# Performance work log

Measured on AMD Instinct MI355X. Metric: run time of the kernel, lower is better.

Reference implementation:

```python
import jax, jax.numpy as jnp
import numpy as np

WINDOW = 4
EPS = 1e-5


def setup_inputs() -> dict:
    key = jax.random.key(0)
    ks = jax.random.split(key, 12)
    B, T, D = 2, 4096, 1024
    H = D // 2
    s = 0.02
    return {
        "x": jax.random.normal(ks[0], (B, T, D), dtype=jnp.float32),
        # tension_net: Linear(2D -> D/2), SiLU, Linear(D/2 -> 1). Weights stored [in, out].
        "w1": jax.random.normal(ks[1], (2 * D, H), dtype=jnp.float32) * s,
        "b1": jnp.zeros((H,), dtype=jnp.float32),
        "w2": jax.random.normal(ks[2], (H, 1), dtype=jnp.float32) * s,
        "b2": jnp.zeros((1,), dtype=jnp.float32),
        # wv: Linear(D -> D)
        "wv_w": jax.random.normal(ks[3], (D, D), dtype=jnp.float32) * s,
        "wv_b": jnp.zeros((D,), dtype=jnp.float32),
        # merge: Linear(2D -> D)
        "merge_w": jax.random.normal(ks[4], (2 * D, D), dtype=jnp.float32) * s,
        "merge_b": jnp.zeros((D,), dtype=jnp.float32),
        # LayerNorm(D)
        "gamma": jnp.ones((D,), dtype=jnp.float32),
        "beta": jnp.zeros((D,), dtype=jnp.float32),
    }


def reference(x, w1, b1, w2, b2, wv_w, wv_b, merge_w, merge_b, gamma, beta):
    B, T, D = x.shape
    W = WINDOW
    # Causal sliding-window neighbor gather: nb[:, t, w] = x[:, t-w-1] if t-w-1 >= 0 else 0.
    idx = jnp.arange(T)[:, None] - jnp.arange(W)[None, :] - 1          # [T, W]
    valid = (idx >= 0)                                                  # [T, W]
    nb = jnp.take(x, jnp.clip(idx, 0, None), axis=1)                   # [B, T, W, D]
    nb = jnp.where(valid[None, :, :, None], nb, jnp.zeros((), x.dtype))
    # Pairwise tension gate: tiny MLP on [h_t, nb].
    h_t = jnp.broadcast_to(x[:, :, None, :], (B, T, W, D))
    pair = jnp.concatenate([h_t, nb], axis=-1)                          # [B, T, W, 2D]
    hid = jax.nn.silu(jnp.einsum('btwe,eh->btwh', pair, w1) + b1)       # [B, T, W, D/2]
    tau = jax.nn.sigmoid((jnp.einsum('btwh,ho->btwo', hid, w2) + b2)[..., 0])  # [B, T, W]
    # Value projection of neighbors (note: zero-padded neighbors still get wv bias, matching torch).
    v = jnp.einsum('btwd,de->btwe', nb, wv_w) + wv_b                    # [B, T, W, D]
    msg = jnp.einsum('btw,btwd->btd', tau, v)                           # [B, T, D]
    # Merge + LayerNorm.
    y = jnp.einsum('bte,ed->btd', jnp.concatenate([x, msg], axis=-1), merge_w) + merge_b
    mu = jnp.mean(y, axis=-1, keepdims=True)
    var = jnp.mean(jnp.square(y - mu), axis=-1, keepdims=True)
    y = (y - mu) * jax.lax.rsqrt(var + EPS) * gamma + beta
    return y
```

## Files before the change

### kernel.cpp

```cpp
#include <hip/hip_runtime.h>
#include <hip/hip_bf16.h>

#define TT 4096
#define TD 1024
#define TH 512
#define TM 8192
#define EPS 1e-5f

typedef __bf16 bf16;
typedef __bf16 bf16x2 __attribute__((ext_vector_type(2)));
typedef __bf16 bf16x4 __attribute__((ext_vector_type(4)));
typedef __bf16 bf16x8 __attribute__((ext_vector_type(8)));
typedef float  f32x4  __attribute__((ext_vector_type(4)));

#define GLOBAL_AS __attribute__((address_space(1)))
#define LDS_AS    __attribute__((address_space(3)))

__global__ __launch_bounds__(256) void cast_x_kernel(const float4* __restrict__ x4,
                                                     bf16* __restrict__ XM) {
    int i = blockIdx.x * 256 + threadIdx.x;
    float4 v = x4[i];
    int row = i >> 8;
    int c4  = i & 255;
    bf16x4 o;
    o[0] = (bf16)v.x; o[1] = (bf16)v.y; o[2] = (bf16)v.z; o[3] = (bf16)v.w;
    *(bf16x4*)(XM + (size_t)row * 2048 + c4 * 4) = o;
}

__global__ __launch_bounds__(256) void transpose_w1wv(const float* __restrict__ w1,
                                                      const float* __restrict__ wv,
                                                      bf16* __restrict__ dst) {
    __shared__ float tile[32][33];
    const int z = blockIdx.z;
    const float* src; int N, dstOff;
    if (z == 0)      { src = w1;                      N = 512;  dstOff = 0;    }
    else if (z == 1) { src = w1 + (size_t)1024 * 512; N = 512;  dstOff = 512;  }
    else             { src = wv;                      N = 1024; dstOff = 1024; }
    int n0 = blockIdx.x * 32, k0 = blockIdx.y * 32;
    if (n0 >= N) return;
    int tx = threadIdx.x & 31, ty = threadIdx.x >> 5;
#pragma unroll
    for (int r = 0; r < 32; r += 8)
        tile[ty + r][tx] = src[(size_t)(k0 + ty + r) * N + n0 + tx];
    __syncthreads();
#pragma unroll
    for (int r = 0; r < 32; r += 8)
        dst[(size_t)(dstOff + n0 + ty + r) * 1024 + k0 + tx] = (bf16)tile[tx][ty + r];
}

__global__ __launch_bounds__(256) void transpose_merge(const float* __restrict__ src,
                                                       bf16* __restrict__ dst) {
    __shared__ float tile[32][33];
    int n0 = blockIdx.x * 32, k0 = blockIdx.y * 32;
    int tx = threadIdx.x & 31, ty = threadIdx.x >> 5;
#pragma unroll
    for (int r = 0; r < 32; r += 8)
        tile[ty + r][tx] = src[(size_t)(k0 + ty + r) * 1024 + n0 + tx];
    __syncthreads();
#pragma unroll
    for (int r = 0; r < 32; r += 8)
        dst[(size_t)(n0 + ty + r) * 2048 + k0 + tx] = (bf16)tile[tx][ty + r];
}

template <typename OutT>
__global__ __launch_bounds__(256) void gemm_bt(const bf16* __restrict__ A, int lda,
                                               const bf16* __restrict__ BT,
                                               OutT* __restrict__ C, int N, int K) {
    __shared__ bf16 As[128 * 64];
    __shared__ bf16 Bs[128 * 64];
    const int m0 = blockIdx.y * 128;
    const int n0 = blockIdx.x * 128;
    const int tid = threadIdx.x;
    const int wave = tid >> 6, lane = tid & 63;
    const int wr = (wave >> 1) * 64, wc = (wave & 1) * 64;
    const int lrow = lane & 15, cbase = lane >> 4;
    const int sw = lrow & 7;

    f32x4 acc[4][4] = {};

    for (int k0 = 0; k0 < K; k0 += 64) {
        __syncthreads();
#pragma unroll
        for (int c = 0; c < 4; ++c) {
            int e = (c * 256 + tid) * 8;
            int row = e >> 6;
            int q = (e >> 3) & 7;
            int gcol = ((q ^ (row & 7)) << 3);
            const bf16* ga = A  + (size_t)(m0 + row) * lda + k0 + gcol;
            const bf16* gb = BT + (size_t)(n0 + row) * K   + k0 + gcol;
            __builtin_amdgcn_global_load_lds((const GLOBAL_AS void*)ga,
                                             (LDS_AS void*)(As + e), 16, 0, 0);
            __builtin_amdgcn_global_load_lds((const GLOBAL_AS void*)gb,
                                             (LDS_AS void*)(Bs + e), 16, 0, 0);
        }
        __syncthreads();

#pragma unroll
        for (int kk = 0; kk < 2; ++kk) {
            const int qo = ((cbase + kk * 4) ^ sw) << 3;
            bf16x8 af[4], bfr[4];
#pragma unroll
            for (int i = 0; i < 4; ++i) {
                af[i]  = *(const bf16x8*)(As + (wr + i * 16 + lrow) * 64 + qo);
                bfr[i] = *(const bf16x8*)(Bs + (wc + i * 16 + lrow) * 64 + qo);
            }
#pragma unroll
            for (int i = 0; i < 4; ++i)
#pragma unroll
                for (int j = 0; j < 4; ++j)
                    acc[i][j] = __builtin_amdgcn_mfma_f32_16x16x32_bf16(af[i], bfr[j], acc[i][j], 0, 0, 0);
        }
    }

    const int lr = (lane >> 4) * 4, lc = lane & 15;
#pragma unroll
    for (int i = 0; i < 4; ++i)
#pragma unroll
        for (int j = 0; j < 4; ++j)
#pragma unroll
            for (int r = 0; r < 4; ++r)
                C[(size_t)(m0 + wr + i * 16 + lr + r) * N + (n0 + wc + j * 16 + lc)]
                    = (OutT)acc[i][j][r];
}

__global__ __launch_bounds__(256) void taumsg_kernel(const bf16* __restrict__ UVV,
                                                     const float* __restrict__ b1,
                                                     const float* __restrict__ b2,
                                                     const float* __restrict__ w2,
                                                     const float* __restrict__ wv_b,
                                                     bf16* __restrict__ XM) {
    const int row = blockIdx.x;
    const int t = row & (TT - 1);
    const int tid = threadIdx.x;

    const int h = tid * 2;
    bf16x2 ub = *(const bf16x2*)(UVV + (size_t)row * 2048 + h);
    float u0 = (float)ub[0] + b1[h];
    float u1 = (float)ub[1] + b1[h + 1];
    const float w20 = w2[h], w21 = w2[h + 1];

    float partial[4];
#pragma unroll
    for (int w = 0; w < 4; ++w) {
        float vn0 = 0.f, vn1 = 0.f;
        if (t >= w + 1) {
            bf16x2 vb = *(const bf16x2*)(UVV + (size_t)(row - w - 1) * 2048 + 512 + h);
            vn0 = (float)vb[0]; vn1 = (float)vb[1];
        }
        float z0 = u0 + vn0, z1 = u1 + vn1;
        float h0 = z0 / (1.f + __expf(-z0));
        float h1 = z1 / (1.f + __expf(-z1));
        partial[w] = h0 * w20 + h1 * w21;
    }
#pragma unroll
    for (int w = 0; w < 4; ++w)
        for (int off = 32; off; off >>= 1)
            partial[w] += __shfl_down(partial[w], off, 64);

    __shared__ float red[4][4];
    __shared__ float staus[4];
    const int lane = tid & 63, wave = tid >> 6;
    if (lane == 0)
#pragma unroll
        for (int w = 0; w < 4; ++w) red[w][wave] = partial[w];
    __syncthreads();
    if (tid < 4) {
        float s = red[tid][0] + red[tid][1] + red[tid][2] + red[tid][3] + b2[0];
        staus[tid] = 1.f / (1.f + __expf(-s));
    }
    __syncthreads();
    const float tau0 = staus[0], tau1 = staus[1], tau2 = staus[2], tau3 = staus[3];
    const float tsum = tau0 + tau1 + tau2 + tau3;

    const int d0 = tid * 4;
    float4 wb = *(const float4*)(wv_b + d0);
    float m[4] = {tsum * wb.x, tsum * wb.y, tsum * wb.z, tsum * wb.w};
    const float taus[4] = {tau0, tau1, tau2, tau3};
#pragma unroll
    for (int w = 0; w < 4; ++w) {
        if (t >= w + 1) {
            bf16x4 v = *(const bf16x4*)(UVV + (size_t)(row - w - 1) * 2048 + 1024 + d0);
#pragma unroll
            for (int j = 0; j < 4; ++j) m[j] += taus[w] * (float)v[j];
        }
    }
    bf16x4 o;
#pragma unroll
    for (int j = 0; j < 4; ++j) o[j] = (bf16)m[j];
    *(bf16x4*)(XM + (size_t)row * 2048 + 1024 + d0) = o;
}

__global__ __launch_bounds__(256) void ln_kernel(const bf16* __restrict__ Y,
                                                 const float* __restrict__ merge_b,
                                                 const float* __restrict__ gamma,
                                                 const float* __restrict__ beta,
                                                 float* __restrict__ out) {
    const int row = blockIdx.x;
    const int tid = threadIdx.x;
    const int d0 = tid * 4;
    bf16x4 y4 = *(const bf16x4*)(Y + (size_t)row * TD + d0);
    float4 mb = *(const float4*)(merge_b + d0);
    float v[4] = {(float)y4[0] + mb.x, (float)y4[1] + mb.y,
                  (float)y4[2] + mb.z, (float)y4[3] + mb.w};
    float s = v[0] + v[1] + v[2] + v[3];
    float ss = v[0]*v[0] + v[1]*v[1] + v[2]*v[2] + v[3]*v[3];
    for (int off = 32; off; off >>= 1) {
        s  += __shfl_down(s, off, 64);
        ss += __shfl_down(ss, off, 64);
    }
    __shared__ float rs[4], rss[4];
    __shared__ float smu, srstd;
    const int lane = tid & 63, wave = tid >> 6;
    if (lane == 0) { rs[wave] = s; rss[wave] = ss; }
    __syncthreads();
    if (tid == 0) {
        float S = rs[0] + rs[1] + rs[2] + rs[3];
        float SS = rss[0] + rss[1] + rss[2] + rss[3];
        float mu = S * (1.f / TD);
        float var = SS * (1.f / TD) - mu * mu;
        smu = mu; srstd = rsqrtf(var + EPS);
    }
    __syncthreads();
    const float mu = smu, r = srstd;
    float4 g = *(const float4*)(gamma + d0);
    float4 bt = *(const float4*)(beta + d0);
    float4 o;
    o.x = (v[0] - mu) * r * g.x + bt.x;
    o.y = (v[1] - mu) * r * g.y + bt.y;
    o.z = (v[2] - mu) * r * g.z + bt.z;
    o.w = (v[3] - mu) * r * g.w + bt.w;
    *(float4*)(out + (size_t)row * TD + d0) = o;
}

extern "C" void kernel_launch(void* const* d_in, const int* in_sizes, int n_in,
                              void* d_out, int out_size, void* d_ws, size_t ws_size,
                              hipStream_t stream) {
    const float* x       = (const float*)d_in[0];
    const float* w1      = (const float*)d_in[1];
    const float* b1      = (const float*)d_in[2];
    const float* w2      = (const float*)d_in[3];
    const float* b2      = (const float*)d_in[4];
    const float* wv_w    = (const float*)d_in[5];
    const float* wv_b    = (const float*)d_in[6];
    const float* merge_w = (const float*)d_in[7];
    const float* merge_b = (const float*)d_in[8];
    const float* gamma   = (const float*)d_in[9];
    const float* beta    = (const float*)d_in[10];
    float* out = (float*)d_out;

    char* ws = (char*)d_ws;
    bf16*  XM     = (bf16*)ws;   ws += (size_t)TM * 2048 * 2;
    bf16*  WbigT  = (bf16*)ws;   ws += (size_t)2048 * 1024 * 2;
    bf16*  MergeT = (bf16*)ws;   ws += (size_t)1024 * 2048 * 2;
    bf16*  UVV    = (bf16*)ws;   ws += (size_t)TM * 2048 * 2;
    bf16*  Y      = (bf16*)ws;

    cast_x_kernel<<<TM * TD / 4 / 256, 256, 0, stream>>>((const float4*)x, XM);

    transpose_w1wv<<<dim3(32, 32, 3), 256, 0, stream>>>(w1, wv_w, WbigT);
    transpose_merge<<<dim3(32, 64), 256, 0, stream>>>(merge_w, MergeT);

    gemm_bt<bf16><<<dim3(2048 / 128, TM / 128), 256, 0, stream>>>(XM, 2048, WbigT, UVV, 2048, 1024);

    taumsg_kernel<<<TM, 256, 0, stream>>>(UVV, b1, b2, w2, wv_b, XM);

    gemm_bt<bf16><<<dim3(1024 / 128, TM / 128), 256, 0, stream>>>(XM, 2048, MergeT, Y, 1024, 2048);

    ln_kernel<<<TM, 256, 0, stream>>>(Y, merge_b, gamma, beta, out);
}
```

Before: 236.1 us.

## Fold value projection into merge weights and fuse tau/message with LayerNorm

Uses the linearity of msg @ merge_w[D:] to precompute Wv·Mb and the bias vector wv_b·Mb. One 8192×3072×1024 GEMM then yields the gate inputs and per-token partial outputs, which the final kernel combines with tau weights over the window and normalizes. This removes the second K=2048 GEMM, the msg round-trip through global memory and separate cast/transpose/LN launches. It also adds XCD-aware block swizzling and a small weight-product GEMM. Trade-off: the weight product is rounded to bf16, and intermediate C rows hold bf16 partial sums.

```diff
diff --git a/kernel.cpp b/kernel.cpp
--- a/kernel.cpp
+++ b/kernel.cpp
@@ -3,8 +3,8 @@
 
 #define TT 4096
 #define TD 1024
-#define TH 512
 #define TM 8192
+#define CN 3072
 #define EPS 1e-5f
 
 typedef __bf16 bf16;
@@ -16,60 +16,79 @@
 #define GLOBAL_AS __attribute__((address_space(1)))
 #define LDS_AS    __attribute__((address_space(3)))
 
-__global__ __launch_bounds__(256) void cast_x_kernel(const float4* __restrict__ x4,
-                                                     bf16* __restrict__ XM) {
-    int i = blockIdx.x * 256 + threadIdx.x;
-    float4 v = x4[i];
-    int row = i >> 8;
-    int c4  = i & 255;
-    bf16x4 o;
-    o[0] = (bf16)v.x; o[1] = (bf16)v.y; o[2] = (bf16)v.z; o[3] = (bf16)v.w;
-    *(bf16x4*)(XM + (size_t)row * 2048 + c4 * 4) = o;
-}
-
-__global__ __launch_bounds__(256) void transpose_w1wv(const float* __restrict__ w1,
-                                                      const float* __restrict__ wv,
-                                                      bf16* __restrict__ dst) {
+__global__ __launch_bounds__(256) void prep_kernel(const float* __restrict__ x,
+                                                   const float* __restrict__ w1,
+                                                   const float* __restrict__ wv_w,
+                                                   const float* __restrict__ wv_b,
+                                                   const float* __restrict__ merge_w,
+                                                   bf16* __restrict__ Xbf,
+                                                   bf16* __restrict__ BigBT,
+                                                   bf16* __restrict__ Amb,
+                                                   bf16* __restrict__ WvBf,
+                                                   float* __restrict__ cvec) {
     __shared__ float tile[32][33];
-    const int z = blockIdx.z;
-    const float* src; int N, dstOff;
-    if (z == 0)      { src = w1;                      N = 512;  dstOff = 0;    }
-    else if (z == 1) { src = w1 + (size_t)1024 * 512; N = 512;  dstOff = 512;  }
-    else             { src = wv;                      N = 1024; dstOff = 1024; }
-    int n0 = blockIdx.x * 32, k0 = blockIdx.y * 32;
-    if (n0 >= N) return;
-    int tx = threadIdx.x & 31, ty = threadIdx.x >> 5;
+    int b = blockIdx.x;
+    const int tid = threadIdx.x;
+
+    if (b < 4) {
+        int j = b * 256 + tid;
+        const float* col = merge_w + (size_t)1024 * 1024 + j;
+        float acc = 0.f;
+#pragma unroll 16
+        for (int e = 0; e < 1024; ++e) acc += wv_b[e] * col[(size_t)e * 1024];
+        cvec[j] = acc;
+        return;
+    }
+    b -= 4;
+    if (b < 8192) {
+        int i = b * 256 + tid;
+        float4 v = ((const float4*)x)[i];
+        bf16x4 o; o[0] = (bf16)v.x; o[1] = (bf16)v.y; o[2] = (bf16)v.z; o[3] = (bf16)v.w;
+        *(bf16x4*)(Xbf + (size_t)i * 4) = o;
+        return;
+    }
+    b -= 8192;
+
+    const float* src; bf16* dst; int srcN, tilesX, dstOff;
+    if (b < 512)       {           src = w1;                        srcN = 512;  tilesX = 16; dst = BigBT; dstOff = 0;    }
+    else if (b < 1024) { b -= 512; src = w1 + (size_t)1024 * 512;   srcN = 512;  tilesX = 16; dst = BigBT; dstOff = 512;  }
+    else if (b < 2048) { b -= 1024; src = merge_w;                  srcN = 1024; tilesX = 32; dst = BigBT; dstOff = 2048; }
+    else if (b < 3072) { b -= 2048; src = merge_w + (size_t)1024 * 1024; srcN = 1024; tilesX = 32; dst = Amb; dstOff = 0; }
+    else {
+        b -= 3072;
+        int i = b * 256 + tid;
+        float4 v = ((const float4*)wv_w)[i];
+        bf16x4 o; o[0] = (bf16)v.x; o[1] = (bf16)v.y; o[2] = (bf16)v.z; o[3] = (bf16)v.w;
+        *(bf16x4*)(WvBf + (size_t)i * 4) = o;
+        return;
+    }
+    int n0 = (b % tilesX) * 32, k0 = (b / tilesX) * 32;
+    int tx = tid & 31, ty = tid >> 5;
 #pragma unroll
     for (int r = 0; r < 32; r += 8)
-        tile[ty + r][tx] = src[(size_t)(k0 + ty + r) * N + n0 + tx];
+        tile[ty + r][tx] = src[(size_t)(k0 + ty + r) * srcN + n0 + tx];
     __syncthreads();
 #pragma unroll
     for (int r = 0; r < 32; r += 8)
         dst[(size_t)(dstOff + n0 + ty + r) * 1024 + k0 + tx] = (bf16)tile[tx][ty + r];
 }
 
-__global__ __launch_bounds__(256) void transpose_merge(const float* __restrict__ src,
-                                                       bf16* __restrict__ dst) {
-    __shared__ float tile[32][33];
-    int n0 = blockIdx.x * 32, k0 = blockIdx.y * 32;
-    int tx = threadIdx.x & 31, ty = threadIdx.x >> 5;
-#pragma unroll
-    for (int r = 0; r < 32; r += 8)
-        tile[ty + r][tx] = src[(size_t)(k0 + ty + r) * 1024 + n0 + tx];
-    __syncthreads();
-#pragma unroll
-    for (int r = 0; r < 32; r += 8)
-        dst[(size_t)(n0 + ty + r) * 2048 + k0 + tx] = (bf16)tile[tx][ty + r];
-}
-
-template <typename OutT>
+template <typename OutT, bool SWIZ>
 __global__ __launch_bounds__(256) void gemm_bt(const bf16* __restrict__ A, int lda,
                                                const bf16* __restrict__ BT,
                                                OutT* __restrict__ C, int N, int K) {
     __shared__ bf16 As[128 * 64];
     __shared__ bf16 Bs[128 * 64];
-    const int m0 = blockIdx.y * 128;
-    const int n0 = blockIdx.x * 128;
+    int bx = blockIdx.x, by = blockIdx.y;
+    if (SWIZ) {
+        int L = by * gridDim.x + bx;
+        int xcd = L & 7, idx = L >> 3;
+        int nyx = gridDim.y >> 3;
+        by = xcd * nyx + idx / gridDim.x;
+        bx = idx % gridDim.x;
+    }
+    const int m0 = by * 128;
+    const int n0 = bx * 128;
     const int tid = threadIdx.x;
     const int wave = tid >> 6, lane = tid & 63;
     const int wr = (wave >> 1) * 64, wc = (wave & 1) * 64;
@@ -123,34 +142,39 @@
                     = (OutT)acc[i][j][r];
 }
 
-__global__ __launch_bounds__(256) void taumsg_kernel(const bf16* __restrict__ UVV,
-                                                     const float* __restrict__ b1,
-                                                     const float* __restrict__ b2,
-                                                     const float* __restrict__ w2,
-                                                     const float* __restrict__ wv_b,
-                                                     bf16* __restrict__ XM) {
+__global__ __launch_bounds__(256) void final_kernel(const bf16* __restrict__ C,
+                                                    const float* __restrict__ b1,
+                                                    const float* __restrict__ b2,
+                                                    const float* __restrict__ w2,
+                                                    const float* __restrict__ cvec,
+                                                    const float* __restrict__ merge_b,
+                                                    const float* __restrict__ gamma,
+                                                    const float* __restrict__ beta,
+                                                    float* __restrict__ out) {
     const int row = blockIdx.x;
     const int t = row & (TT - 1);
     const int tid = threadIdx.x;
+    const bf16* Crow = C + (size_t)row * CN;
 
     const int h = tid * 2;
-    bf16x2 ub = *(const bf16x2*)(UVV + (size_t)row * 2048 + h);
-    float u0 = (float)ub[0] + b1[h];
-    float u1 = (float)ub[1] + b1[h + 1];
-    const float w20 = w2[h], w21 = w2[h + 1];
+    bf16x2 u2 = *(const bf16x2*)(Crow + h);
+    float2 b1v = *(const float2*)(b1 + h);
+    float2 w2v = *(const float2*)(w2 + h);
+    const float u0 = (float)u2[0] + b1v.x;
+    const float u1 = (float)u2[1] + b1v.y;
 
     float partial[4];
 #pragma unroll
     for (int w = 0; w < 4; ++w) {
         float vn0 = 0.f, vn1 = 0.f;
         if (t >= w + 1) {
-            bf16x2 vb = *(const bf16x2*)(UVV + (size_t)(row - w - 1) * 2048 + 512 + h);
-            vn0 = (float)vb[0]; vn1 = (float)vb[1];
+            bf16x2 v2 = *(const bf16x2*)(C + (size_t)(row - w - 1) * CN + 512 + h);
+            vn0 = (float)v2[0]; vn1 = (float)v2[1];
         }
         float z0 = u0 + vn0, z1 = u1 + vn1;
         float h0 = z0 / (1.f + __expf(-z0));
         float h1 = z1 / (1.f + __expf(-z1));
-        partial[w] = h0 * w20 + h1 * w21;
+        partial[w] = h0 * w2v.x + h1 * w2v.y;
     }
 #pragma unroll
     for (int w = 0; w < 4; ++w)
@@ -171,37 +195,25 @@
     __syncthreads();
     const float tau0 = staus[0], tau1 = staus[1], tau2 = staus[2], tau3 = staus[3];
     const float tsum = tau0 + tau1 + tau2 + tau3;
+    const float taus[4] = {tau0, tau1, tau2, tau3};
 
     const int d0 = tid * 4;
-    float4 wb = *(const float4*)(wv_b + d0);
-    float m[4] = {tsum * wb.x, tsum * wb.y, tsum * wb.z, tsum * wb.w};
-    const float taus[4] = {tau0, tau1, tau2, tau3};
+    bf16x4 y1 = *(const bf16x4*)(Crow + 2048 + d0);
+    float4 cv = *(const float4*)(cvec + d0);
+    float4 mb = *(const float4*)(merge_b + d0);
+    float v[4] = {(float)y1[0] + tsum * cv.x + mb.x,
+                  (float)y1[1] + tsum * cv.y + mb.y,
+                  (float)y1[2] + tsum * cv.z + mb.z,
+                  (float)y1[3] + tsum * cv.w + mb.w};
 #pragma unroll
     for (int w = 0; w < 4; ++w) {
         if (t >= w + 1) {
-            bf16x4 v = *(const bf16x4*)(UVV + (size_t)(row - w - 1) * 2048 + 1024 + d0);
-#pragma unroll
-            for (int j = 0; j < 4; ++j) m[j] += taus[w] * (float)v[j];
-        }
-    }
-    bf16x4 o;
-#pragma unroll
-    for (int j = 0; j < 4; ++j) o[j] = (bf16)m[j];
-    *(bf16x4*)(XM + (size_t)row * 2048 + 1024 + d0) = o;
-}
-
-__global__ __launch_bounds__(256) void ln_kernel(const bf16* __restrict__ Y,
-                                                 const float* __restrict__ merge_b,
-                                                 const float* __restrict__ gamma,
-                                                 const float* __restrict__ beta,
-                                                 float* __restrict__ out) {
-    const int row = blockIdx.x;
-    const int tid = threadIdx.x;
-    const int d0 = tid * 4;
-    bf16x4 y4 = *(const bf16x4*)(Y + (size_t)row * TD + d0);
-    float4 mb = *(const float4*)(merge_b + d0);
-    float v[4] = {(float)y4[0] + mb.x, (float)y4[1] + mb.y,
-                  (float)y4[2] + mb.z, (float)y4[3] + mb.w};
+            bf16x4 p = *(const bf16x4*)(C + (size_t)(row - w - 1) * CN + 1024 + d0);
+#pragma unroll
+            for (int j = 0; j < 4; ++j) v[j] += taus[w] * (float)p[j];
+        }
+    }
+
     float s = v[0] + v[1] + v[2] + v[3];
     float ss = v[0]*v[0] + v[1]*v[1] + v[2]*v[2] + v[3]*v[3];
     for (int off = 32; off; off >>= 1) {
@@ -210,7 +222,6 @@
     }
     __shared__ float rs[4], rss[4];
     __shared__ float smu, srstd;
-    const int lane = tid & 63, wave = tid >> 6;
     if (lane == 0) { rs[wave] = s; rss[wave] = ss; }
     __syncthreads();
     if (tid == 0) {
@@ -222,7 +233,7 @@
     }
     __syncthreads();
     const float mu = smu, r = srstd;
-    float4 g = *(const float4*)(gamma + d0);
+    float4 g  = *(const float4*)(gamma + d0);
     float4 bt = *(const float4*)(beta + d0);
     float4 o;
     o.x = (v[0] - mu) * r * g.x + bt.x;
@@ -249,22 +260,22 @@
     float* out = (float*)d_out;
 
     char* ws = (char*)d_ws;
-    bf16*  XM     = (bf16*)ws;   ws += (size_t)TM * 2048 * 2;
-    bf16*  WbigT  = (bf16*)ws;   ws += (size_t)2048 * 1024 * 2;
-    bf16*  MergeT = (bf16*)ws;   ws += (size_t)1024 * 2048 * 2;
-    bf16*  UVV    = (bf16*)ws;   ws += (size_t)TM * 2048 * 2;
-    bf16*  Y      = (bf16*)ws;
-
-    cast_x_kernel<<<TM * TD / 4 / 256, 256, 0, stream>>>((const float4*)x, XM);
-
-    transpose_w1wv<<<dim3(32, 32, 3), 256, 0, stream>>>(w1, wv_w, WbigT);
-    transpose_merge<<<dim3(32, 64), 256, 0, stream>>>(merge_w, MergeT);
-
-    gemm_bt<bf16><<<dim3(2048 / 128, TM / 128), 256, 0, stream>>>(XM, 2048, WbigT, UVV, 2048, 1024);
-
-    taumsg_kernel<<<TM, 256, 0, stream>>>(UVV, b1, b2, w2, wv_b, XM);
-
-    gemm_bt<bf16><<<dim3(1024 / 128, TM / 128), 256, 0, stream>>>(XM, 2048, MergeT, Y, 1024, 2048);
-
-    ln_kernel<<<TM, 256, 0, stream>>>(Y, merge_b, gamma, beta, out);
-}
+    bf16*  Xbf   = (bf16*)ws;  ws += (size_t)TM * 1024 * 2;
+    bf16*  BigBT = (bf16*)ws;  ws += (size_t)CN * 1024 * 2;
+    bf16*  Amb   = (bf16*)ws;  ws += (size_t)1024 * 1024 * 2;
+    bf16*  WvBf  = (bf16*)ws;  ws += (size_t)1024 * 1024 * 2;
+    float* cvec  = (float*)ws; ws += (size_t)1024 * 4;
+    bf16*  Cbuf  = (bf16*)ws;
+
+    prep_kernel<<<12292, 256, 0, stream>>>(x, w1, wv_w, wv_b, merge_w,
+                                           Xbf, BigBT, Amb, WvBf, cvec);
+
+    gemm_bt<bf16, false><<<dim3(8, 8), 256, 0, stream>>>(
+        Amb, 1024, WvBf, BigBT + (size_t)1024 * 1024, 1024, 1024);
+
+    gemm_bt<bf16, true><<<dim3(CN / 128, TM / 128), 256, 0, stream>>>(
+        Xbf, 1024, BigBT, Cbuf, CN, 1024);
+
+    final_kernel<<<TM, 256, 0, stream>>>(Cbuf, b1, b2, w2, cvec, merge_b,
+                                         gamma, beta, out);
+}
```

New measurement: 242.1 us. 2.5% more time.
